# Optimization experiments

Measured on AMD Instinct MI355X. Metric: run time of the kernel, lower is better.

The kernel has to match this reference:

```python
import jax, jax.numpy as jnp
import numpy as np

IN_DIM = 512

def setup_inputs() -> dict:
    key = jax.random.key(0)
    ks = jax.random.split(key, 7)
    s = 1.0 / np.sqrt(IN_DIM)
    x = jax.random.normal(ks[0], (8, 2048, IN_DIM), dtype=jnp.float32)
    Wq = jax.random.uniform(ks[1], (IN_DIM, IN_DIM), jnp.float32, -s, s)
    bq = jax.random.uniform(ks[2], (IN_DIM,), jnp.float32, -s, s)
    Wk = jax.random.uniform(ks[3], (IN_DIM, IN_DIM), jnp.float32, -s, s)
    bk = jax.random.uniform(ks[4], (IN_DIM,), jnp.float32, -s, s)
    Wv = jax.random.uniform(ks[5], (IN_DIM, IN_DIM), jnp.float32, -s, s)
    bv = jax.random.uniform(ks[6], (IN_DIM,), jnp.float32, -s, s)
    return {"x": x, "Wq": Wq, "bq": bq, "Wk": Wk, "bk": bk, "Wv": Wv, "bv": bv}

def reference(x, Wq, bq, Wk, bk, Wv, bv):
    # Q,K,V projections: torch Linear is x @ W.T + b; Wq here is [out,in]
    q = jnp.einsum('bsc,dc->bsd', x, Wq) + bq
    k = jnp.einsum('bsc,dc->bsd', x, Wk) + bk
    v = jnp.einsum('bsc,dc->bsd', x, Wv) + bv
    energy = jnp.einsum('bqd,bkd->bqk', q, k)  # no scaling, matches source
    attention = jax.nn.softmax(energy, axis=-1)
    out = jnp.einsum('bqk,bkd->bqd', attention, v)
    return out
```

## Files before the change

kernel.cpp:

```cpp
#include <hip/hip_runtime.h>

typedef unsigned short u16;
typedef _Float16 f16;

using half8   = __attribute__((ext_vector_type(8))) _Float16;
using f32x4   = __attribute__((ext_vector_type(4))) float;
using ushort8 = __attribute__((ext_vector_type(8))) unsigned short;
using us4     = __attribute__((ext_vector_type(4))) unsigned short;
using float4v = __attribute__((ext_vector_type(4))) float;

#define B_  8
#define S_  2048
#define D_  512
#define BK  64

__device__ __forceinline__ u16 f2h(float f) {
  f16 h = (f16)f;
  u16 u;
  __builtin_memcpy(&u, &h, 2);
  return u;
}

__device__ __forceinline__ float h2f(u16 h) {
  f16 x;
  __builtin_memcpy(&x, &h, 2);
  return (float)x;
}

__device__ __forceinline__ void stage16(const void* g, void* l) {
  __builtin_amdgcn_global_load_lds((const __attribute__((address_space(1))) void*)g,
                                   (__attribute__((address_space(3))) void*)l,
                                   16, 0, 0);
}

__device__ __forceinline__ void xcd_remap(int& bx, int& by, int& bz) {
  const int lin = ((int)blockIdx.z * (int)gridDim.y + (int)blockIdx.y) * (int)gridDim.x
                  + (int)blockIdx.x;
  const int nwg = (int)gridDim.x * (int)gridDim.y * (int)gridDim.z;
  const int swz = (lin & 7) * (nwg >> 3) + (lin >> 3);
  bx = swz % (int)gridDim.x;
  const int tmp = swz / (int)gridDim.x;
  by = tmp % (int)gridDim.y;
  bz = tmp / (int)gridDim.y;
}

__device__ __forceinline__ void gemm_core(const u16* __restrict__ A, const u16* __restrict__ B,
                                          int K, int m0, int n0,
                                          u16* ldsA, u16* ldsB, f32x4 acc[4][4]) {
  const int tid  = threadIdx.x;
  const int lane = tid & 63;
  const int wave = tid >> 6;
  const int wr = wave >> 1, wc = wave & 1;
  const int srow = wave * 8 + (lane >> 3);
  const int scol = (((lane & 7) ^ (lane >> 3)) << 3);
  const int fr   = lane & 15;
  const int fgrp = lane >> 4;

  const f32x4 vzero = {0.f, 0.f, 0.f, 0.f};
  #pragma unroll
  for (int m = 0; m < 4; ++m)
    #pragma unroll
    for (int n = 0; n < 4; ++n)
      acc[m][n] = vzero;

  const int T = K / BK;
  const u16* gA = A + (size_t)(m0 + srow) * K + scol;
  const u16* gB = B + (size_t)(n0 + srow) * K + scol;

  int cur = 0;
  #pragma unroll
  for (int s = 0; s < 4; ++s) {
    stage16(gA + (size_t)s * 32 * K, ldsA + (s * 32 + wave * 8) * BK);
    stage16(gB + (size_t)s * 32 * K, ldsB + (s * 32 + wave * 8) * BK);
  }
  __syncthreads();

  for (int t = 0; t < T; ++t) {
    if (t + 1 < T) {
      const u16* pa = gA + (size_t)(t + 1) * BK;
      const u16* pb = gB + (size_t)(t + 1) * BK;
      u16* la = ldsA + (cur ^ 1) * (128 * BK);
      u16* lb = ldsB + (cur ^ 1) * (128 * BK);
      #pragma unroll
      for (int s = 0; s < 4; ++s) {
        stage16(pa + (size_t)s * 32 * K, la + (s * 32 + wave * 8) * BK);
        stage16(pb + (size_t)s * 32 * K, lb + (s * 32 + wave * 8) * BK);
      }
    }
    const u16* la = ldsA + cur * (128 * BK);
    const u16* lb = ldsB + cur * (128 * BK);
    #pragma unroll
    for (int kk = 0; kk < 2; ++kk) {
      const int ce = ((((kk << 2) | fgrp) ^ (fr & 7)) << 3);
      half8 a[4], b[4];
      #pragma unroll
      for (int m = 0; m < 4; ++m)
        a[m] = *(const half8*)(la + (wr * 64 + m * 16 + fr) * BK + ce);
      #pragma unroll
      for (int n = 0; n < 4; ++n)
        b[n] = *(const half8*)(lb + (wc * 64 + n * 16 + fr) * BK + ce);
      #pragma unroll
      for (int m = 0; m < 4; ++m)
        #pragma unroll
        for (int n = 0; n < 4; ++n)
          acc[m][n] = __builtin_amdgcn_mfma_f32_16x16x32_f16(a[m], b[n], acc[m][n], 0, 0, 0);
    }
    __syncthreads();
    cur ^= 1;
  }
}

__global__ __launch_bounds__(256) void proj_kernel(
    const u16* __restrict__ xh, const u16* __restrict__ Wh,
    const float* __restrict__ bq, const float* __restrict__ bk, const float* __restrict__ bv,
    u16* __restrict__ Qb, u16* __restrict__ Kb, u16* __restrict__ Vt) {
  __shared__ __align__(16) u16 ldsA[2 * 128 * BK];
  __shared__ __align__(16) u16 ldsB[2 * 128 * BK];
  int bx, by, bz;
  xcd_remap(bx, by, bz);
  const int z  = bz;
  const int m0 = by * 128;
  const int n0 = bx * 128;
  const u16* W = Wh + (size_t)z * D_ * D_;
  const float* bias = (z == 0) ? bq : (z == 1) ? bk : bv;
  f32x4 acc[4][4];
  gemm_core(xh, W, D_, m0, n0, ldsA, ldsB, acc);

  const int lane = threadIdx.x & 63;
  const int wave = threadIdx.x >> 6;
  const int wr = wave >> 1, wc = wave & 1;
  #pragma unroll
  for (int m = 0; m < 4; ++m) {
    const int gr0 = m0 + wr * 64 + m * 16 + ((lane >> 4) << 2);
    #pragma unroll
    for (int n = 0; n < 4; ++n) {
      const int gc = n0 + wc * 64 + n * 16 + (lane & 15);
      const float bb = bias[gc];
      if (z < 2) {
        u16* O = z ? Kb : Qb;
        #pragma unroll
        for (int r = 0; r < 4; ++r)
          O[(size_t)(gr0 + r) * D_ + gc] = f2h(acc[m][n][r] + bb);
      } else {
        const int bidx = gr0 >> 11;
        const int s    = gr0 & 2047;
        us4 p;
        #pragma unroll
        for (int r = 0; r < 4; ++r) p[r] = f2h(acc[m][n][r] + bb);
        *(us4*)(Vt + ((size_t)bidx * D_ + gc) * S_ + s) = p;
      }
    }
  }
}

__global__ __launch_bounds__(256) void qk_kernel(
    const u16* __restrict__ Qb, const u16* __restrict__ Kb, u16* __restrict__ E,
    size_t sA, size_t sE) {
  __shared__ __align__(16) u16 ldsA[2 * 128 * BK];
  __shared__ __align__(16) u16 ldsB[2 * 128 * BK];
  int bx, by, bz;
  xcd_remap(bx, by, bz);
  const int z  = bz;
  const int m0 = by * 128;
  const int n0 = bx * 128;
  f32x4 acc[4][4];
  gemm_core(Qb + (size_t)z * sA, Kb + (size_t)z * sA, D_, m0, n0, ldsA, ldsB, acc);

  u16* Eb = E + (size_t)z * sE;
  const int lane = threadIdx.x & 63;
  const int wave = threadIdx.x >> 6;
  const int wr = wave >> 1, wc = wave & 1;
  #pragma unroll
  for (int m = 0; m < 4; ++m) {
    const int gr0 = m0 + wr * 64 + m * 16 + ((lane >> 4) << 2);
    #pragma unroll
    for (int n = 0; n < 4; ++n) {
      const int gc = n0 + wc * 64 + n * 16 + (lane & 15);
      #pragma unroll
      for (int r = 0; r < 4; ++r)
        Eb[(size_t)(gr0 + r) * S_ + gc] = f2h(acc[m][n][r]);
    }
  }
}

__global__ __launch_bounds__(256) void softmax_kernel(u16* __restrict__ E) {
  const int row  = blockIdx.x * 4 + (threadIdx.x >> 6);
  const int lane = threadIdx.x & 63;
  u16* R = E + (size_t)row * S_;
  float e[32];
  #pragma unroll
  for (int i = 0; i < 4; ++i) {
    ushort8 v = *(const ushort8*)(R + i * 512 + lane * 8);
    #pragma unroll
    for (int j = 0; j < 8; ++j) e[i * 8 + j] = h2f(v[j]);
  }
  float m = e[0];
  #pragma unroll
  for (int i = 1; i < 32; ++i) m = fmaxf(m, e[i]);
  for (int off = 32; off > 0; off >>= 1) m = fmaxf(m, __shfl_xor(m, off, 64));
  float s = 0.f;
  #pragma unroll
  for (int i = 0; i < 32; ++i) { e[i] = __expf(e[i] - m); s += e[i]; }
  for (int off = 32; off > 0; off >>= 1) s += __shfl_xor(s, off, 64);
  const float inv = 1.f / s;
  #pragma unroll
  for (int i = 0; i < 4; ++i) {
    ushort8 v;
    #pragma unroll
    for (int j = 0; j < 8; ++j) v[j] = f2h(e[i * 8 + j] * inv);
    *(ushort8*)(R + i * 512 + lane * 8) = v;
  }
}

__global__ __launch_bounds__(256) void pv_kernel(
    const u16* __restrict__ P, const u16* __restrict__ Vt, float* __restrict__ out,
    size_t sP, size_t sV, size_t sO) {
  __shared__ __align__(16) u16 ldsA[2 * 128 * BK];
  __shared__ __align__(16) u16 ldsB[2 * 128 * BK];
  int bx, by, bz;
  xcd_remap(bx, by, bz);
  const int z  = bz;
  const int m0 = by * 128;
  const int n0 = bx * 128;
  f32x4 acc[4][4];
  gemm_core(P + (size_t)z * sP, Vt + (size_t)z * sV, S_, m0, n0, ldsA, ldsB, acc);

  float* Ob = out + (size_t)z * sO;
  const int lane = threadIdx.x & 63;
  const int wave = threadIdx.x >> 6;
  const int wr = wave >> 1, wc = wave & 1;
  #pragma unroll
  for (int m = 0; m < 4; ++m) {
    const int gr0 = m0 + wr * 64 + m * 16 + ((lane >> 4) << 2);
    #pragma unroll
    for (int n = 0; n < 4; ++n) {
      const int gc = n0 + wc * 64 + n * 16 + (lane & 15);
      #pragma unroll
      for (int r = 0; r < 4; ++r)
        Ob[(size_t)(gr0 + r) * D_ + gc] = acc[m][n][r];
    }
  }
}

__global__ __launch_bounds__(256) void cvt_kernel(const float* __restrict__ in,
                                                  u16* __restrict__ out, int n8) {
  const int i = blockIdx.x * 256 + threadIdx.x;
  if (i >= n8) return;
  const float4v a = *(const float4v*)(in + (size_t)i * 8);
  const float4v b = *(const float4v*)(in + (size_t)i * 8 + 4);
  ushort8 o;
  o[0] = f2h(a[0]); o[1] = f2h(a[1]); o[2] = f2h(a[2]); o[3] = f2h(a[3]);
  o[4] = f2h(b[0]); o[5] = f2h(b[1]); o[6] = f2h(b[2]); o[7] = f2h(b[3]);
  *(ushort8*)(out + (size_t)i * 8) = o;
}

extern "C" void kernel_launch(void* const* d_in, const int* in_sizes, int n_in,
                              void* d_out, int out_size, void* d_ws, size_t ws_size,
                              hipStream_t stream) {
  (void)in_sizes; (void)n_in; (void)out_size;
  const float* x  = (const float*)d_in[0];
  const float* Wq = (const float*)d_in[1];
  const float* bq = (const float*)d_in[2];
  const float* Wk = (const float*)d_in[3];
  const float* bk = (const float*)d_in[4];
  const float* Wv = (const float*)d_in[5];
  const float* bv = (const float*)d_in[6];
  float* out = (float*)d_out;

  char* ws = (char*)d_ws;
  size_t off = 0;
  auto alloc = [&](size_t bytes) -> char* {
    char* p = ws + off;
    off += (bytes + 255) & ~(size_t)255;
    return p;
  };
  const size_t MS = (size_t)B_ * S_;
  u16* xh = (u16*)alloc(MS * D_ * 2);
  u16* Wh = (u16*)alloc(3ull * D_ * D_ * 2);
  u16* Qb = (u16*)alloc(MS * D_ * 2);
  u16* Kb = (u16*)alloc(MS * D_ * 2);
  u16* Vt = (u16*)alloc(MS * D_ * 2);
  const size_t Efull = (size_t)B_ * S_ * S_ * 2;
  const bool full = ws_size >= off + Efull;
  u16* E = (u16*)alloc(full ? Efull : (size_t)S_ * S_ * 2);

  {
    const int n8 = (int)(MS * D_ / 8);
    cvt_kernel<<<dim3((n8 + 255) / 256), dim3(256), 0, stream>>>(x, xh, n8);
    const int w8 = D_ * D_ / 8;
    cvt_kernel<<<dim3((w8 + 255) / 256), dim3(256), 0, stream>>>(Wq, Wh, w8);
    cvt_kernel<<<dim3((w8 + 255) / 256), dim3(256), 0, stream>>>(Wk, Wh + D_ * D_, w8);
    cvt_kernel<<<dim3((w8 + 255) / 256), dim3(256), 0, stream>>>(Wv, Wh + 2 * D_ * D_, w8);
  }

  proj_kernel<<<dim3(D_ / 128, MS / 128, 3), dim3(256), 0, stream>>>(
      xh, Wh, bq, bk, bv, Qb, Kb, Vt);

  if (full) {
    qk_kernel<<<dim3(S_ / 128, S_ / 128, B_), dim3(256), 0, stream>>>(
        Qb, Kb, E, (size_t)S_ * D_, (size_t)S_ * S_);
    softmax_kernel<<<dim3(B_ * S_ / 4), dim3(256), 0, stream>>>(E);
    pv_kernel<<<dim3(D_ / 128, S_ / 128, B_), dim3(256), 0, stream>>>(
        E, Vt, out, (size_t)S_ * S_, (size_t)D_ * S_, (size_t)S_ * D_);
  } else {
    for (int b = 0; b < B_; ++b) {
      qk_kernel<<<dim3(S_ / 128, S_ / 128, 1), dim3(256), 0, stream>>>(
          Qb + (size_t)b * S_ * D_, Kb + (size_t)b * S_ * D_, E, 0, 0);
      softmax_kernel<<<dim3(S_ / 4), dim3(256), 0, stream>>>(E);
      pv_kernel<<<dim3(D_ / 128, S_ / 128, 1), dim3(256), 0, stream>>>(
          E, Vt + (size_t)b * D_ * S_, out + (size_t)b * S_ * D_, 0, 0, 0);
    }
  }
}
```

Baseline: 170.1 us.

## Deepen GEMM pipeline to 4-stage with BK=32 and merge weight conversions

Rewrites the shared GEMM core to use a K-step of 32 and a 4-buffer ring in LDS, with three tiles prefetched ahead and a single barrier per iteration gated by explicit vmcnt waits. It uses a new swizzled LDS layout, precomputed fragment offsets, and raises wave priority around the MFMA block. This is meant to hide global-load latency better and remove one barrier per step, at the cost of twice as many iterations and the same total LDS. The three weight-conversion launches are also merged into one kernel to cut launch overhead.

```diff
diff --git a/kernel.cpp b/kernel.cpp
--- a/kernel.cpp
+++ b/kernel.cpp
@@ -12,7 +12,9 @@
 #define B_  8
 #define S_  2048
 #define D_  512
-#define BK  64
+#define BK  32
+#define TILE_ELEMS 4096
+#define BUF_ELEMS  8192
 
 __device__ __forceinline__ u16 f2h(float f) {
   f16 h = (f16)f;
@@ -46,16 +48,36 @@
 
 __device__ __forceinline__ void gemm_core(const u16* __restrict__ A, const u16* __restrict__ B,
                                           int K, int m0, int n0,
-                                          u16* ldsA, u16* ldsB, f32x4 acc[4][4]) {
+                                          u16* lds, f32x4 acc[4][4]) {
   const int tid  = threadIdx.x;
   const int lane = tid & 63;
   const int wave = tid >> 6;
   const int wr = wave >> 1, wc = wave & 1;
-  const int srow = wave * 8 + (lane >> 3);
-  const int scol = (((lane & 7) ^ (lane >> 3)) << 3);
   const int fr   = lane & 15;
   const int fgrp = lane >> 4;
 
+  int sr[2], sc[2];
+  #pragma unroll
+  for (int s = 0; s < 2; ++s) {
+    const int p    = tid * 16 + s * 4096;
+    const int R    = p >> 7;
+    const int slot = (p >> 4) & 7;
+    const int s0   = slot ^ (R & 7);
+    sr[s] = 2 * R + (s0 >> 2);
+    sc[s] = (s0 & 3) * 8;
+  }
+
+  int offA[4], offB[4];
+  #pragma unroll
+  for (int m = 0; m < 4; ++m) {
+    const int ra = wr * 64 + m * 16 + fr;
+    const int Ra = ra >> 1;
+    offA[m] = Ra * 128 + (((((ra & 1) << 2) | fgrp) ^ (Ra & 7)) << 4);
+    const int rb = wc * 64 + m * 16 + fr;
+    const int Rb = rb >> 1;
+    offB[m] = Rb * 128 + (((((rb & 1) << 2) | fgrp) ^ (Rb & 7)) << 4);
+  }
+
   const f32x4 vzero = {0.f, 0.f, 0.f, 0.f};
   #pragma unroll
   for (int m = 0; m < 4; ++m)
@@ -64,58 +86,55 @@
       acc[m][n] = vzero;
 
   const int T = K / BK;
-  const u16* gA = A + (size_t)(m0 + srow) * K + scol;
-  const u16* gB = B + (size_t)(n0 + srow) * K + scol;
-
-  int cur = 0;
-  #pragma unroll
-  for (int s = 0; s < 4; ++s) {
-    stage16(gA + (size_t)s * 32 * K, ldsA + (s * 32 + wave * 8) * BK);
-    stage16(gB + (size_t)s * 32 * K, ldsB + (s * 32 + wave * 8) * BK);
-  }
-  __syncthreads();
-
-  for (int t = 0; t < T; ++t) {
-    if (t + 1 < T) {
-      const u16* pa = gA + (size_t)(t + 1) * BK;
-      const u16* pb = gB + (size_t)(t + 1) * BK;
-      u16* la = ldsA + (cur ^ 1) * (128 * BK);
-      u16* lb = ldsB + (cur ^ 1) * (128 * BK);
-      #pragma unroll
-      for (int s = 0; s < 4; ++s) {
-        stage16(pa + (size_t)s * 32 * K, la + (s * 32 + wave * 8) * BK);
-        stage16(pb + (size_t)s * 32 * K, lb + (s * 32 + wave * 8) * BK);
-      }
-    }
-    const u16* la = ldsA + cur * (128 * BK);
-    const u16* lb = ldsB + cur * (128 * BK);
-    #pragma unroll
-    for (int kk = 0; kk < 2; ++kk) {
-      const int ce = ((((kk << 2) | fgrp) ^ (fr & 7)) << 3);
-      half8 a[4], b[4];
-      #pragma unroll
-      for (int m = 0; m < 4; ++m)
-        a[m] = *(const half8*)(la + (wr * 64 + m * 16 + fr) * BK + ce);
-      #pragma unroll
-      for (int n = 0; n < 4; ++n)
-        b[n] = *(const half8*)(lb + (wc * 64 + n * 16 + fr) * BK + ce);
-      #pragma unroll
-      for (int m = 0; m < 4; ++m)
-        #pragma unroll
-        for (int n = 0; n < 4; ++n)
-          acc[m][n] = __builtin_amdgcn_mfma_f32_16x16x32_f16(a[m], b[n], acc[m][n], 0, 0, 0);
-    }
-    __syncthreads();
-    cur ^= 1;
-  }
+
+  auto STAGE = [&](int t, u16* buf) {
+    #pragma unroll
+    for (int s = 0; s < 2; ++s) {
+      stage16(A + (size_t)(m0 + sr[s]) * K + t * BK + sc[s],
+              buf + s * 2048 + wave * 512);
+      stage16(B + (size_t)(n0 + sr[s]) * K + t * BK + sc[s],
+              buf + TILE_ELEMS + s * 2048 + wave * 512);
+    }
+  };
+
+  STAGE(0, lds);
+  STAGE(1, lds + BUF_ELEMS);
+  STAGE(2, lds + 2 * BUF_ELEMS);
+
+  int t = 0;
+#define GEMM_ITER(WN)                                                            \
+  {                                                                              \
+    asm volatile("s_waitcnt vmcnt(" #WN ")\n\ts_barrier" ::: "memory");          \
+    const u16* buf = lds + (t & 3) * BUF_ELEMS;                                  \
+    half8 a[4], b[4];                                                            \
+    _Pragma("unroll")                                                            \
+    for (int m = 0; m < 4; ++m)                                                  \
+      a[m] = *(const half8*)((const char*)buf + offA[m]);                        \
+    _Pragma("unroll")                                                            \
+    for (int n = 0; n < 4; ++n)                                                  \
+      b[n] = *(const half8*)((const char*)(buf + TILE_ELEMS) + offB[n]);         \
+    if (t + 3 < T) STAGE(t + 3, lds + ((t + 3) & 3) * BUF_ELEMS);                \
+    __builtin_amdgcn_s_setprio(1);                                               \
+    _Pragma("unroll")                                                            \
+    for (int m = 0; m < 4; ++m)                                                  \
+      _Pragma("unroll")                                                          \
+      for (int n = 0; n < 4; ++n)                                                \
+        acc[m][n] = __builtin_amdgcn_mfma_f32_16x16x32_f16(a[m], b[n],           \
+                                                           acc[m][n], 0, 0, 0); \
+    __builtin_amdgcn_s_setprio(0);                                               \
+  }
+
+  for (; t < T - 2; ++t) GEMM_ITER(8)
+  GEMM_ITER(4); ++t;
+  GEMM_ITER(0);
+#undef GEMM_ITER
 }
 
 __global__ __launch_bounds__(256) void proj_kernel(
     const u16* __restrict__ xh, const u16* __restrict__ Wh,
     const float* __restrict__ bq, const float* __restrict__ bk, const float* __restrict__ bv,
     u16* __restrict__ Qb, u16* __restrict__ Kb, u16* __restrict__ Vt) {
-  __shared__ __align__(16) u16 ldsA[2 * 128 * BK];
-  __shared__ __align__(16) u16 ldsB[2 * 128 * BK];
+  __shared__ __align__(16) u16 lds[4 * BUF_ELEMS];
   int bx, by, bz;
   xcd_remap(bx, by, bz);
   const int z  = bz;
@@ -124,7 +143,7 @@
   const u16* W = Wh + (size_t)z * D_ * D_;
   const float* bias = (z == 0) ? bq : (z == 1) ? bk : bv;
   f32x4 acc[4][4];
-  gemm_core(xh, W, D_, m0, n0, ldsA, ldsB, acc);
+  gemm_core(xh, W, D_, m0, n0, lds, acc);
 
   const int lane = threadIdx.x & 63;
   const int wave = threadIdx.x >> 6;
@@ -156,15 +175,14 @@
 __global__ __launch_bounds__(256) void qk_kernel(
     const u16* __restrict__ Qb, const u16* __restrict__ Kb, u16* __restrict__ E,
     size_t sA, size_t sE) {
-  __shared__ __align__(16) u16 ldsA[2 * 128 * BK];
-  __shared__ __align__(16) u16 ldsB[2 * 128 * BK];
+  __shared__ __align__(16) u16 lds[4 * BUF_ELEMS];
   int bx, by, bz;
   xcd_remap(bx, by, bz);
   const int z  = bz;
   const int m0 = by * 128;
   const int n0 = bx * 128;
   f32x4 acc[4][4];
-  gemm_core(Qb + (size_t)z * sA, Kb + (size_t)z * sA, D_, m0, n0, ldsA, ldsB, acc);
+  gemm_core(Qb + (size_t)z * sA, Kb + (size_t)z * sA, D_, m0, n0, lds, acc);
 
   u16* Eb = E + (size_t)z * sE;
   const int lane = threadIdx.x & 63;
@@ -215,15 +233,14 @@
 __global__ __launch_bounds__(256) void pv_kernel(
     const u16* __restrict__ P, const u16* __restrict__ Vt, float* __restrict__ out,
     size_t sP, size_t sV, size_t sO) {
-  __shared__ __align__(16) u16 ldsA[2 * 128 * BK];
-  __shared__ __align__(16) u16 ldsB[2 * 128 * BK];
+  __shared__ __align__(16) u16 lds[4 * BUF_ELEMS];
   int bx, by, bz;
   xcd_remap(bx, by, bz);
   const int z  = bz;
   const int m0 = by * 128;
   const int n0 = bx * 128;
   f32x4 acc[4][4];
-  gemm_core(P + (size_t)z * sP, Vt + (size_t)z * sV, S_, m0, n0, ldsA, ldsB, acc);
+  gemm_core(P + (size_t)z * sP, Vt + (size_t)z * sV, S_, m0, n0, lds, acc);
 
   float* Ob = out + (size_t)z * sO;
   const int lane = threadIdx.x & 63;
@@ -252,6 +269,22 @@
   o[0] = f2h(a[0]); o[1] = f2h(a[1]); o[2] = f2h(a[2]); o[3] = f2h(a[3]);
   o[4] = f2h(b[0]); o[5] = f2h(b[1]); o[6] = f2h(b[2]); o[7] = f2h(b[3]);
   *(ushort8*)(out + (size_t)i * 8) = o;
+}
+
+__global__ __launch_bounds__(256) void cvt3_kernel(const float* __restrict__ w0,
+                                                   const float* __restrict__ w1,
+                                                   const float* __restrict__ w2,
+                                                   u16* __restrict__ out, int n8) {
+  const int i = blockIdx.x * 256 + threadIdx.x;
+  if (i >= n8) return;
+  const float* in = (blockIdx.y == 0) ? w0 : (blockIdx.y == 1) ? w1 : w2;
+  u16* o_ = out + (size_t)blockIdx.y * D_ * D_;
+  const float4v a = *(const float4v*)(in + (size_t)i * 8);
+  const float4v b = *(const float4v*)(in + (size_t)i * 8 + 4);
+  ushort8 o;
+  o[0] = f2h(a[0]); o[1] = f2h(a[1]); o[2] = f2h(a[2]); o[3] = f2h(a[3]);
+  o[4] = f2h(b[0]); o[5] = f2h(b[1]); o[6] = f2h(b[2]); o[7] = f2h(b[3]);
+  *(ushort8*)(o_ + (size_t)i * 8) = o;
 }
 
 extern "C" void kernel_launch(void* const* d_in, const int* in_sizes, int n_in,
@@ -288,9 +321,7 @@
     const int n8 = (int)(MS * D_ / 8);
     cvt_kernel<<<dim3((n8 + 255) / 256), dim3(256), 0, stream>>>(x, xh, n8);
     const int w8 = D_ * D_ / 8;
-    cvt_kernel<<<dim3((w8 + 255) / 256), dim3(256), 0, stream>>>(Wq, Wh, w8);
-    cvt_kernel<<<dim3((w8 + 255) / 256), dim3(256), 0, stream>>>(Wk, Wh + D_ * D_, w8);
-    cvt_kernel<<<dim3((w8 + 255) / 256), dim3(256), 0, stream>>>(Wv, Wh + 2 * D_ * D_, w8);
+    cvt3_kernel<<<dim3((w8 + 255) / 256, 3), dim3(256), 0, stream>>>(Wq, Wk, Wv, Wh, w8);
   }
 
   proj_kernel<<<dim3(D_ / 128, MS / 128, 3), dim3(256), 0, stream>>>(
```

Measured after the change: 160.6 us. 5.6% less time.
